# Kernel optimization log

Hardware: AMD Instinct MI355X
Metric: run time of the kernel (lower is better)

Reference implementation:

```python
import jax, jax.numpy as jnp
import numpy as np
import math

DEPTH = 12
LAMBDA_INIT = 0.8 - 0.6 * math.exp(-0.3 * DEPTH)
EPS = 1e-5


def setup_inputs() -> dict:
    key = jax.random.key(0)
    ks = jax.random.split(key, 10)
    B, S, E, H, D = 2, 2048, 1024, 8, 64
    query = jax.random.normal(ks[0], (B, S, E), dtype=jnp.float32)
    init = 0.02
    Wq = jax.random.normal(ks[1], (E, 2 * H * D), dtype=jnp.float32) * init
    Wk = jax.random.normal(ks[2], (E, 2 * H * D), dtype=jnp.float32) * init
    Wv = jax.random.normal(ks[3], (E, 2 * H * D), dtype=jnp.float32) * init
    Wo = jax.random.normal(ks[4], (2 * H * D, E), dtype=jnp.float32) * init
    lq1 = jax.random.normal(ks[5], (D,), dtype=jnp.float32) * 0.1
    lk1 = jax.random.normal(ks[6], (D,), dtype=jnp.float32) * 0.1
    lq2 = jax.random.normal(ks[7], (D,), dtype=jnp.float32) * 0.1
    lk2 = jax.random.normal(ks[8], (D,), dtype=jnp.float32) * 0.1
    subln_w = jnp.ones((2 * D,), dtype=jnp.float32)
    return {"query": query, "Wq": Wq, "Wk": Wk, "Wv": Wv, "Wo": Wo,
            "lq1": lq1, "lk1": lk1, "lq2": lq2, "lk2": lk2, "subln_w": subln_w}


def reference(query, Wq, Wk, Wv, Wo, lq1, lk1, lq2, lk2, subln_w):
    B, S, E = query.shape
    D = lq1.shape[0]
    H = Wq.shape[1] // (2 * D)
    scaling = D ** -0.5
    # projections -> (B, 2H, S, D) for q/k, (B, H, S, 2D) for v
    q = (query @ Wq).reshape(B, S, 2 * H, D).transpose(0, 2, 1, 3) * scaling
    k = (query @ Wk).reshape(B, S, 2 * H, D).transpose(0, 2, 1, 3)
    v = (query @ Wv).reshape(B, S, H, 2 * D).transpose(0, 2, 1, 3)
    score = jnp.einsum('bhqd,bhkd->bhqk', q, k)  # (B, 2H, S, S)
    score = jnp.nan_to_num(score)
    score = jax.nn.softmax(score.astype(jnp.float32), axis=-1).astype(score.dtype)
    lambda_1 = jnp.exp(jnp.sum(lq1 * lk1))
    lambda_2 = jnp.exp(jnp.sum(lq2 * lk2))
    lambda_full = lambda_1 - lambda_2 + LAMBDA_INIT
    score = score.reshape(B, H, 2, S, S)
    score = score[:, :, 0] - lambda_full * score[:, :, 1]  # (B, H, S, S)
    attn = jnp.einsum('bhqk,bhkd->bhqd', score, v)  # (B, H, S, 2D)
    # RMSNorm over last dim (computed in fp32, cast back), affine weight
    af = attn.astype(jnp.float32)
    attn = (af * jax.lax.rsqrt(jnp.mean(af * af, axis=-1, keepdims=True) + EPS)).astype(attn.dtype)
    attn = attn * subln_w
    attn = attn * (1.0 - LAMBDA_INIT)
    attn = attn.transpose(0, 2, 1, 3).reshape(B, S, H * 2 * D)
    return attn @ Wo
```

## Files before the change

kernel.cpp:

```cpp
#include <hip/hip_runtime.h>

typedef __attribute__((ext_vector_type(4))) float f32x4;
typedef __attribute__((ext_vector_type(8))) short bf16x8;
typedef unsigned short u16;
typedef unsigned int u32;

#define LAMBDA_INIT 0.7836057665311429f
#define ONE_MINUS_LI 0.2163942334688571f
#define QSCALE_LOG2 0.1803368801111137f

__device__ __forceinline__ u16 f2b(float f){
  union { float f; unsigned u; } v; v.f = f;
  unsigned r = v.u + 0x7fff + ((v.u >> 16) & 1);
  return (u16)(r >> 16);
}

__device__ __forceinline__ f32x4 mfma16(bf16x8 a, bf16x8 b, f32x4 c){
  return __builtin_amdgcn_mfma_f32_16x16x32_bf16(a, b, c, 0, 0, 0);
}

__device__ __forceinline__ float exp2_raw(float x){
  float r;
  asm("v_exp_f32 %0, %1" : "=v"(r) : "v"(x));
  return r;
}

__device__ __forceinline__ void async16(void* lds, const void* g){
  __builtin_amdgcn_global_load_lds((const __attribute__((address_space(1))) void*)g,
                                   (__attribute__((address_space(3))) void*)lds, 16, 0, 0);
}

__global__ void prep(const float* __restrict__ query,
                     const float* __restrict__ Wq, const float* __restrict__ Wk,
                     const float* __restrict__ Wv, const float* __restrict__ Wo,
                     u16* __restrict__ Xbf, u16* __restrict__ Wqkvt, u16* __restrict__ Wot){
  int z = blockIdx.z;
  int tx = threadIdx.x, ty = threadIdx.y;
  if (z == 4){
    int bidf = blockIdx.y * 32 + blockIdx.x;
    int t = ty * 32 + tx;
    const float4* in4 = (const float4*)query;
    ushort4* out4 = (ushort4*)Xbf;
    #pragma unroll
    for (int k = 0; k < 4; k++){
      int i = bidf * 1024 + k * 256 + t;
      float4 f = in4[i];
      ushort4 o; o.x = f2b(f.x); o.y = f2b(f.y); o.z = f2b(f.z); o.w = f2b(f.w);
      out4[i] = o;
    }
    return;
  }
  __shared__ float t[32][33];
  int c0 = blockIdx.x * 32, r0 = blockIdx.y * 32;
  const float* in = (z == 0) ? Wq : (z == 1) ? Wk : (z == 2) ? Wv : Wo;
  u16* out = (z < 3) ? (Wqkvt + (size_t)z * 1048576) : Wot;
  for (int i = 0; i < 32; i += 8) t[ty + i][tx] = in[(size_t)(r0 + ty + i) * 1024 + c0 + tx];
  __syncthreads();
  for (int i = 0; i < 32; i += 8) out[(size_t)(c0 + ty + i) * 1024 + r0 + tx] = f2b(t[tx][ty + i]);
}

template<int PERM>
__global__ void transpose_bf16(const u16* __restrict__ in, u16* __restrict__ out, int R, int C){
  __shared__ u16 t[32][34];
  int c0 = blockIdx.x * 32, r0 = blockIdx.y * 32;
  size_t boff = (size_t)blockIdx.z * R * C;
  int tx = threadIdx.x, ty = threadIdx.y;
  for (int i = 0; i < 32; i += 8) t[ty + i][tx] = in[boff + (size_t)(r0 + ty + i) * C + c0 + tx];
  __syncthreads();
  for (int i = 0; i < 32; i += 8){
    int dv = c0 + ty + i, s = r0 + tx;
    int sx;
    if (PERM){
      int sl = s & 63;
      int n = sl >> 4, g = (sl >> 2) & 3, r = sl & 3;
      int pos = (s & ~63) | ((n >> 1) << 5) | (g << 3) | ((n & 1) << 2) | r;
      sx = (pos & ~63) | ((((pos >> 3) & 7) ^ (dv & 7)) << 3) | (pos & 7);
    } else sx = s;
    out[boff + (size_t)dv * R + sx] = t[tx][ty + i];
  }
}

template<int BN, int EPI>
__global__ __launch_bounds__(256, 2) void gemm_async(
    const u16* __restrict__ A, const u16* __restrict__ Bt, float* __restrict__ Cp,
    u16* __restrict__ Qo, u16* __restrict__ Ko, u16* __restrict__ Vo,
    int M, int N, int K, int gm){
  constexpr int BCH = BN / 32;
  __shared__ u16 As[2][128 * 64];
  __shared__ u16 Bs[2][BN * 64];
  int tid = threadIdx.x, w = tid >> 6, lane = tid & 63;
  int l16 = lane & 15, grp = lane >> 4;
  int wr = w >> 1, wc = w & 1;
  int nwg = gridDim.x, bid = blockIdx.x;
  int idx = (bid & 7) * (nwg >> 3) + (bid >> 3);
  int m0 = (idx & (gm - 1)) * 128, n0 = (idx / gm) * BN;

  int sr = lane >> 3;
  int sc = ((lane & 7) ^ sr) << 3;
  const u16* pA = A  + (size_t)(m0 + w * 8 + sr) * K + sc;
  const u16* pB = Bt + (size_t)(n0 + w * 8 + sr) * K + sc;

  f32x4 acc[4][BN / 32] = {};

#define STAGEG(bb, k0) do{                                             \
    _Pragma("unroll")                                                  \
    for (int i = 0; i < 4; i++)                                        \
      async16(&As[bb][i * 2048 + w * 512], pA + (k0) + (size_t)i * 32 * K); \
    _Pragma("unroll")                                                  \
    for (int i = 0; i < BCH; i++)                                      \
      async16(&Bs[bb][i * 2048 + w * 512], pB + (k0) + (size_t)i * 32 * K); \
  } while(0)

  STAGEG(0, 0);
  int niter = K >> 6;
  for (int kt = 0; kt < niter; kt++){
    int cur = kt & 1;
    if (kt < niter - 1){
      STAGEG(cur ^ 1, (kt + 1) << 6);
      if constexpr (BN == 128) asm volatile("s_waitcnt vmcnt(8)" ::: "memory");
      else                     asm volatile("s_waitcnt vmcnt(6)" ::: "memory");
    } else {
      asm volatile("s_waitcnt vmcnt(0)" ::: "memory");
    }
    __builtin_amdgcn_s_barrier();

    const u16* Ap = As[cur];
    const u16* Bp = Bs[cur];
    #pragma unroll
    for (int kk = 0; kk < 2; kk++){
      bf16x8 a[4], b[BN / 32];
      #pragma unroll
      for (int m = 0; m < 4; m++){
        int r = wr * 64 + m * 16 + l16;
        a[m] = *(const bf16x8*)&Ap[r * 64 + (((kk * 4 + grp) ^ (r & 7)) << 3)];
      }
      #pragma unroll
      for (int n = 0; n < BCH; n++){
        int r = wc * (BN / 2) + n * 16 + l16;
        b[n] = *(const bf16x8*)&Bp[r * 64 + (((kk * 4 + grp) ^ (r & 7)) << 3)];
      }
      #pragma unroll
      for (int m = 0; m < 4; m++)
        #pragma unroll
        for (int n = 0; n < BCH; n++)
          acc[m][n] = mfma16(a[m], b[n], acc[m][n]);
    }
    if (kt < niter - 1){
      asm volatile("s_waitcnt lgkmcnt(0)" ::: "memory");
      __builtin_amdgcn_s_barrier();
    }
  }
#undef STAGEG

  if constexpr (EPI == 0){
    #pragma unroll
    for (int m = 0; m < 4; m++)
      #pragma unroll
      for (int n = 0; n < BCH; n++)
        #pragma unroll
        for (int r = 0; r < 4; r++)
          Cp[(size_t)(m0 + wr * 64 + m * 16 + grp * 4 + r) * N + n0 + wc * (BN / 2) + n * 16 + l16]
            = acc[m][n][r];
  } else {
    int proj = n0 >> 10;
    #pragma unroll
    for (int m = 0; m < 4; m++){
      int row = m0 + wr * 64 + m * 16 + grp * 4;
      #pragma unroll
      for (int n = 0; n < BCH; n++){
        int col = n0 + wc * (BN / 2) + n * 16 + l16;
        int cn = col & 1023;
        if (proj == 0){
          #pragma unroll
          for (int r = 0; r < 4; r++)
            Qo[(size_t)(row + r) * 1024 + cn] = f2b(acc[m][n][r] * QSCALE_LOG2);
        } else if (proj == 1){
          #pragma unroll
          for (int r = 0; r < 4; r++){
            int cs = (cn & ~63) | ((((cn >> 3) & 7) ^ ((row + r) & 7)) << 3) | (cn & 7);
            Ko[(size_t)(row + r) * 1024 + cs] = f2b(acc[m][n][r]);
          }
        } else {
          #pragma unroll
          for (int r = 0; r < 4; r++)
            Vo[(size_t)(row + r) * 1024 + cn] = f2b(acc[m][n][r]);
        }
      }
    }
  }
}

__global__ __launch_bounds__(256, 2) void diff_attn(
    const u16* __restrict__ Qb, const u16* __restrict__ Kb, const u16* __restrict__ Vt,
    const float* __restrict__ lq1, const float* __restrict__ lk1,
    const float* __restrict__ lq2, const float* __restrict__ lk2,
    const float* __restrict__ slw, u16* __restrict__ attnb){
  __shared__ u16 Ksh[2][2][64 * 64];
  __shared__ u16 Vsh[3][128 * 64];

  int tid = threadIdx.x, w = tid >> 6, lane = tid & 63;
  int l16 = lane & 15, grp = lane >> 4;
  int bid = blockIdx.x;
  int h = bid & 7, qt = (bid >> 3) & 31, b = bid >> 8;
  int tb = b * 2048 + qt * 64;

  float lam;
  {
    float p1 = lq1[lane] * lk1[lane], p2 = lq2[lane] * lk2[lane];
    #pragma unroll
    for (int m = 32; m >= 1; m >>= 1){ p1 += __shfl_xor(p1, m); p2 += __shfl_xor(p2, m); }
    lam = __expf(p1) - __expf(p2) + LAMBDA_INIT;
  }

  const u16* gK1 = Kb + (size_t)(b * 2048 + w * 16 + (lane >> 3)) * 1024 + 128 * h + (lane & 7) * 8;
  const u16* gK2 = gK1 + 64;
  const u16* gV  = Vt + (size_t)(b * 1024 + 128 * h + w * 32 + (lane >> 3)) * 2048 + (lane & 7) * 8;

  bf16x8 q1[2], q2[2];
  {
    const u16* qr = Qb + (size_t)(tb + w * 16 + l16) * 1024 + 128 * h;
    q1[0] = *(const bf16x8*)(qr + grp * 8);
    q1[1] = *(const bf16x8*)(qr + 32 + grp * 8);
    q2[0] = *(const bf16x8*)(qr + 64 + grp * 8);
    q2[1] = *(const bf16x8*)(qr + 96 + grp * 8);
  }

  bf16x8 ones;
  #pragma unroll
  for (int i = 0; i < 8; i++) ones[i] = (short)0x3F80;

#define STAGE_K(bb, PK1, PK2) do{                           \
    async16(&Ksh[bb][0][w * 1024],       (PK1));            \
    async16(&Ksh[bb][0][w * 1024 + 512], (PK1) + 8192);     \
    async16(&Ksh[bb][1][w * 1024],       (PK2));            \
    async16(&Ksh[bb][1][w * 1024 + 512], (PK2) + 8192);     \
  } while(0)
#define STAGE_V(ss, PV) do{                                 \
    async16(&Vsh[ss][w * 2048],          (PV));             \
    async16(&Vsh[ss][w * 2048 + 512],    (PV) + 16384);     \
    async16(&Vsh[ss][w * 2048 + 1024],   (PV) + 32768);     \
    async16(&Vsh[ss][w * 2048 + 1536],   (PV) + 49152);     \
  } while(0)

  int xo0 = ((grp ^ (l16 & 7)) << 3);
  int xo1 = (((4 + grp) ^ (l16 & 7)) << 3);

#define QKCOMP(bb, S1, S2) do{                                           \
    const u16* K1p = Ksh[bb][0];                                         \
    const u16* K2p = Ksh[bb][1];                                         \
    _Pragma("unroll")                                                    \
    for (int n = 0; n < 4; n++){ S1[n] = (f32x4){0,0,0,0}; S2[n] = (f32x4){0,0,0,0}; } \
    _Pragma("unroll")                                                    \
    for (int n = 0; n < 4; n++){                                         \
      int rb = (n * 16 + l16) << 6;                                      \
      bf16x8 k1a = *(const bf16x8*)&K1p[rb + xo0];                       \
      bf16x8 k1b = *(const bf16x8*)&K1p[rb + xo1];                       \
      bf16x8 k2a = *(const bf16x8*)&K2p[rb + xo0];                       \
      bf16x8 k2b = *(const bf16x8*)&K2p[rb + xo1];                       \
      S1[n] = mfma16(k1a, q1[0], S1[n]);                                 \
      S1[n] = mfma16(k1b, q1[1], S1[n]);                                 \
      S2[n] = mfma16(k2a, q2[0], S2[n]);                                 \
      S2[n] = mfma16(k2b, q2[1], S2[n]);                                 \
    }                                                                    \
  } while(0)

#define EXPPACK(S, PB) do{                                               \
    float p[16];                                                         \
    _Pragma("unroll")                                                    \
    for (int n = 0; n < 4; n++)                                          \
      _Pragma("unroll")                                                  \
      for (int r = 0; r < 4; r++) p[n * 4 + r] = exp2_raw(S[n][r] - 4.0f); \
    union { u32 wd[4]; bf16x8 v; } u0, u1;                               \
    _Pragma("unroll")                                                    \
    for (int j = 0; j < 4; j++){                                         \
      asm("v_cvt_pk_bf16_f32 %0, %1, %2" : "=v"(u0.wd[j]) : "v"(p[2 * j]),     "v"(p[2 * j + 1])); \
      asm("v_cvt_pk_bf16_f32 %0, %1, %2" : "=v"(u1.wd[j]) : "v"(p[8 + 2 * j]), "v"(p[9 + 2 * j])); \
    }                                                                    \
    PB[0] = u0.v; PB[1] = u1.v;                                          \
  } while(0)

  STAGE_K(0, gK1, gK2); STAGE_V(0, gV);
  gK1 += 65536; gK2 += 65536; gV += 64;
  STAGE_K(1, gK1, gK2); STAGE_V(1, gV);
  gK1 += 65536; gK2 += 65536; gV += 64;
  __syncthreads();
  f32x4 s1c[4], s2c[4], s1n[4], s2n[4];
  QKCOMP(0, s1c, s2c);

  f32x4 O1[9] = {}, O2[9] = {};
  int vrd = 0, vst = 2;

  for (int kt = 0; kt < 32; kt++){
    if (kt <= 30) asm volatile("s_waitcnt vmcnt(4) lgkmcnt(0)" ::: "memory");
    else          asm volatile("s_waitcnt vmcnt(0) lgkmcnt(0)" ::: "memory");
    __builtin_amdgcn_s_barrier();

    if (kt < 30){
      STAGE_K(kt & 1, gK1, gK2);
      STAGE_V(vst, gV);
      gK1 += 65536; gK2 += 65536; gV += 64;
    }

    if (kt < 31) QKCOMP((kt & 1) ^ 1, s1n, s2n);
    bf16x8 pbA[2], pbB[2];
    EXPPACK(s1c, pbA);
    EXPPACK(s2c, pbB);

    const u16* Vp = Vsh[vrd];
    __builtin_amdgcn_s_setprio(1);
    #pragma unroll
    for (int kk = 0; kk < 2; kk++){
      int xo = kk ? xo1 : xo0;
      #pragma unroll
      for (int n = 0; n < 8; n++){
        bf16x8 av = *(const bf16x8*)&Vp[((n * 16 + l16) << 6) + xo];
        O1[n] = mfma16(av, pbA[kk], O1[n]);
        O2[n] = mfma16(av, pbB[kk], O2[n]);
      }
      O1[8] = mfma16(ones, pbA[kk], O1[8]);
      O2[8] = mfma16(ones, pbB[kk], O2[8]);
    }
    __builtin_amdgcn_s_setprio(0);

    #pragma unroll
    for (int n = 0; n < 4; n++){ s1c[n] = s1n[n]; s2c[n] = s2n[n]; }
    vrd = (vrd == 2) ? 0 : vrd + 1;
    vst = (vst == 2) ? 0 : vst + 1;
  }
#undef STAGE_K
#undef STAGE_V
#undef QKCOMP
#undef EXPPACK

  float i1 = 1.f / O1[8][0], i2 = lam / O2[8][0];
  float x[8][4], ss = 0.f;
  #pragma unroll
  for (int n = 0; n < 8; n++)
    #pragma unroll
    for (int r = 0; r < 4; r++){
      float v = O1[n][r] * i1 - O2[n][r] * i2;
      x[n][r] = v; ss += v * v;
    }
  ss += __shfl_xor(ss, 16);
  ss += __shfl_xor(ss, 32);
  float ri = rsqrtf(ss * (1.f / 128.f) + 1e-5f);
  int row = tb + w * 16 + l16;
  #pragma unroll
  for (int n = 0; n < 8; n++){
    float4 sw = *(const float4*)&slw[n * 16 + grp * 4];
    ushort4 o;
    o.x = f2b(x[n][0] * ri * sw.x * ONE_MINUS_LI);
    o.y = f2b(x[n][1] * ri * sw.y * ONE_MINUS_LI);
    o.z = f2b(x[n][2] * ri * sw.z * ONE_MINUS_LI);
    o.w = f2b(x[n][3] * ri * sw.w * ONE_MINUS_LI);
    *(ushort4*)&attnb[(size_t)row * 1024 + h * 128 + n * 16 + grp * 4] = o;
  }
}

extern "C" void kernel_launch(void* const* d_in, const int* in_sizes, int n_in,
                              void* d_out, int out_size, void* d_ws, size_t ws_size,
                              hipStream_t stream){
  const float* query = (const float*)d_in[0];
  const float* Wq = (const float*)d_in[1];
  const float* Wk = (const float*)d_in[2];
  const float* Wv = (const float*)d_in[3];
  const float* Wo = (const float*)d_in[4];
  const float* lq1 = (const float*)d_in[5];
  const float* lk1 = (const float*)d_in[6];
  const float* lq2 = (const float*)d_in[7];
  const float* lk2 = (const float*)d_in[8];
  const float* slw = (const float*)d_in[9];

  char* ws = (char*)d_ws;
  u16* Xbf   = (u16*)(ws + 0);
  u16* Wqkvt = (u16*)(ws + 8388608);
  u16* Wot   = (u16*)(ws + 14680064);
  u16* Qbuf  = (u16*)(ws + 16777216);
  u16* Kbuf  = (u16*)(ws + 25165824);
  u16* Vbuf  = (u16*)(ws + 33554432);
  u16* Vtr   = (u16*)(ws + 41943040);
  u16* Attn  = (u16*)(ws + 50331648);

  prep<<<dim3(32, 32, 5), dim3(32, 8), 0, stream>>>(query, Wq, Wk, Wv, Wo,
                                                    Xbf, Wqkvt, Wot);

  gemm_async<128, 1><<<768, 256, 0, stream>>>(Xbf, Wqkvt, nullptr, Qbuf, Kbuf, Vbuf,
                                              4096, 3072, 1024, 32);

  transpose_bf16<1><<<dim3(32, 64, 2), dim3(32, 8), 0, stream>>>(Vbuf, Vtr, 2048, 1024);

  diff_attn<<<512, 256, 0, stream>>>(Qbuf, Kbuf, Vtr, lq1, lk1, lq2, lk2, slw, Attn);

  gemm_async<64, 0><<<512, 256, 0, stream>>>(Attn, Wot, (float*)d_out,
                                             nullptr, nullptr, nullptr,
                                             4096, 1024, 1024, 32);
}
```

Baseline: 131.1 us.

## Restructure attention loop into two-stage ping-pong with double-buffered V

Replaces the triple-buffered V ring and per-iteration register copies with an unrolled-by-two ping-pong loop. K and V each use two shared buffers, with separate barriers and waits so loads for the next tile are issued while QK and PV of the current tile run. This cuts LDS usage, which may allow more blocks per CU, and removes the s1n-to-s1c register moves. In exchange it adds an extra barrier per tile and shortens V prefetch distance, which could expose load latency.

```diff
diff --git a/kernel.cpp b/kernel.cpp
--- a/kernel.cpp
+++ b/kernel.cpp
@@ -196,7 +196,7 @@
     const float* __restrict__ lq2, const float* __restrict__ lk2,
     const float* __restrict__ slw, u16* __restrict__ attnb){
   __shared__ u16 Ksh[2][2][64 * 64];
-  __shared__ u16 Vsh[3][128 * 64];
+  __shared__ u16 Vsh[2][128 * 64];
 
   int tid = threadIdx.x, w = tid >> 6, lane = tid & 63;
   int l16 = lane & 15, grp = lane >> 4;
@@ -229,11 +229,11 @@
   #pragma unroll
   for (int i = 0; i < 8; i++) ones[i] = (short)0x3F80;
 
-#define STAGE_K(bb, PK1, PK2) do{                           \
-    async16(&Ksh[bb][0][w * 1024],       (PK1));            \
-    async16(&Ksh[bb][0][w * 1024 + 512], (PK1) + 8192);     \
-    async16(&Ksh[bb][1][w * 1024],       (PK2));            \
-    async16(&Ksh[bb][1][w * 1024 + 512], (PK2) + 8192);     \
+#define STAGE_K(ss, PK1, PK2) do{                           \
+    async16(&Ksh[ss][0][w * 1024],       (PK1));            \
+    async16(&Ksh[ss][0][w * 1024 + 512], (PK1) + 8192);     \
+    async16(&Ksh[ss][1][w * 1024],       (PK2));            \
+    async16(&Ksh[ss][1][w * 1024 + 512], (PK2) + 8192);     \
   } while(0)
 #define STAGE_V(ss, PV) do{                                 \
     async16(&Vsh[ss][w * 2048],          (PV));             \
@@ -245,9 +245,9 @@
   int xo0 = ((grp ^ (l16 & 7)) << 3);
   int xo1 = (((4 + grp) ^ (l16 & 7)) << 3);
 
-#define QKCOMP(bb, S1, S2) do{                                           \
-    const u16* K1p = Ksh[bb][0];                                         \
-    const u16* K2p = Ksh[bb][1];                                         \
+#define QKCOMP(ss, S1, S2) do{                                           \
+    const u16* K1p = Ksh[ss][0];                                         \
+    const u16* K2p = Ksh[ss][1];                                         \
     _Pragma("unroll")                                                    \
     for (int n = 0; n < 4; n++){ S1[n] = (f32x4){0,0,0,0}; S2[n] = (f32x4){0,0,0,0}; } \
     _Pragma("unroll")                                                    \
@@ -279,58 +279,92 @@
     PB[0] = u0.v; PB[1] = u1.v;                                          \
   } while(0)
 
+#define PVBLOCK(ss, PA, PB) do{                                          \
+    const u16* Vp = Vsh[ss];                                             \
+    __builtin_amdgcn_s_setprio(1);                                       \
+    _Pragma("unroll")                                                    \
+    for (int kk = 0; kk < 2; kk++){                                      \
+      int xo = kk ? xo1 : xo0;                                           \
+      _Pragma("unroll")                                                  \
+      for (int n = 0; n < 8; n++){                                       \
+        bf16x8 av = *(const bf16x8*)&Vp[((n * 16 + l16) << 6) + xo];     \
+        O1[n] = mfma16(av, PA[kk], O1[n]);                               \
+        O2[n] = mfma16(av, PB[kk], O2[n]);                               \
+      }                                                                  \
+      O1[8] = mfma16(ones, PA[kk], O1[8]);                               \
+      O2[8] = mfma16(ones, PB[kk], O2[8]);                               \
+    }                                                                    \
+    __builtin_amdgcn_s_setprio(0);                                       \
+  } while(0)
+
   STAGE_K(0, gK1, gK2); STAGE_V(0, gV);
   gK1 += 65536; gK2 += 65536; gV += 64;
   STAGE_K(1, gK1, gK2); STAGE_V(1, gV);
   gK1 += 65536; gK2 += 65536; gV += 64;
   __syncthreads();
-  f32x4 s1c[4], s2c[4], s1n[4], s2n[4];
-  QKCOMP(0, s1c, s2c);
+  f32x4 sE1[4], sE2[4], sO1[4], sO2[4];
+  QKCOMP(0, sE1, sE2);
+  asm volatile("s_waitcnt lgkmcnt(0)" ::: "memory");
+  __builtin_amdgcn_s_barrier();
 
   f32x4 O1[9] = {}, O2[9] = {};
-  int vrd = 0, vst = 2;
-
-  for (int kt = 0; kt < 32; kt++){
-    if (kt <= 30) asm volatile("s_waitcnt vmcnt(4) lgkmcnt(0)" ::: "memory");
-    else          asm volatile("s_waitcnt vmcnt(0) lgkmcnt(0)" ::: "memory");
+
+  for (int t = 0; t < 15; t++){
+    STAGE_K(0, gK1, gK2);
+    gK1 += 65536; gK2 += 65536;
+    asm volatile("s_waitcnt vmcnt(4)" ::: "memory");
     __builtin_amdgcn_s_barrier();
-
-    if (kt < 30){
-      STAGE_K(kt & 1, gK1, gK2);
-      STAGE_V(vst, gV);
-      gK1 += 65536; gK2 += 65536; gV += 64;
-    }
-
-    if (kt < 31) QKCOMP((kt & 1) ^ 1, s1n, s2n);
+    QKCOMP(1, sO1, sO2);
+    {
+      bf16x8 pbA[2], pbB[2];
+      EXPPACK(sE1, pbA);
+      EXPPACK(sE2, pbB);
+      PVBLOCK(0, pbA, pbB);
+    }
+    asm volatile("s_waitcnt lgkmcnt(0)" ::: "memory");
+    __builtin_amdgcn_s_barrier();
+    STAGE_V(0, gV);
+    gV += 64;
+
+    STAGE_K(1, gK1, gK2);
+    gK1 += 65536; gK2 += 65536;
+    asm volatile("s_waitcnt vmcnt(4)" ::: "memory");
+    __builtin_amdgcn_s_barrier();
+    QKCOMP(0, sE1, sE2);
+    {
+      bf16x8 pbA[2], pbB[2];
+      EXPPACK(sO1, pbA);
+      EXPPACK(sO2, pbB);
+      PVBLOCK(1, pbA, pbB);
+    }
+    asm volatile("s_waitcnt lgkmcnt(0)" ::: "memory");
+    __builtin_amdgcn_s_barrier();
+    STAGE_V(1, gV);
+    gV += 64;
+  }
+
+  asm volatile("s_waitcnt vmcnt(0)" ::: "memory");
+  __builtin_amdgcn_s_barrier();
+  QKCOMP(1, sO1, sO2);
+  {
     bf16x8 pbA[2], pbB[2];
-    EXPPACK(s1c, pbA);
-    EXPPACK(s2c, pbB);
-
-    const u16* Vp = Vsh[vrd];
-    __builtin_amdgcn_s_setprio(1);
-    #pragma unroll
-    for (int kk = 0; kk < 2; kk++){
-      int xo = kk ? xo1 : xo0;
-      #pragma unroll
-      for (int n = 0; n < 8; n++){
-        bf16x8 av = *(const bf16x8*)&Vp[((n * 16 + l16) << 6) + xo];
-        O1[n] = mfma16(av, pbA[kk], O1[n]);
-        O2[n] = mfma16(av, pbB[kk], O2[n]);
-      }
-      O1[8] = mfma16(ones, pbA[kk], O1[8]);
-      O2[8] = mfma16(ones, pbB[kk], O2[8]);
-    }
-    __builtin_amdgcn_s_setprio(0);
-
-    #pragma unroll
-    for (int n = 0; n < 4; n++){ s1c[n] = s1n[n]; s2c[n] = s2n[n]; }
-    vrd = (vrd == 2) ? 0 : vrd + 1;
-    vst = (vst == 2) ? 0 : vst + 1;
+    EXPPACK(sE1, pbA);
+    EXPPACK(sE2, pbB);
+    PVBLOCK(0, pbA, pbB);
+  }
+  asm volatile("s_waitcnt lgkmcnt(0)" ::: "memory");
+  __builtin_amdgcn_s_barrier();
+  {
+    bf16x8 pbA[2], pbB[2];
+    EXPPACK(sO1, pbA);
+    EXPPACK(sO2, pbB);
+    PVBLOCK(1, pbA, pbB);
   }
 #undef STAGE_K
 #undef STAGE_V
 #undef QKCOMP
 #undef EXPPACK
+#undef PVBLOCK
 
   float i1 = 1.f / O1[8][0], i2 = lam / O2[8][0];
   float x[8][4], ss = 0.f;
```

New measurement: 132.4 us. Within noise of the previous version (+1.0%).
